# Performance work log

Measured on AMD Instinct MI355X. Metric: run time of the kernel, lower is better.

The kernel has to match this reference:

```python
import jax, jax.numpy as jnp
from jax import lax
import numpy as np

N_ENT = 50000
N_REL = 500
E = 800000
H = 128
BS = 1024
C = 96
KER = 7
KH, KW = 8, 16  # H = KH*KW
TOPK = 15
FLAT = C * (2 * KH - KER + 1) * (KW - KER + 1)  # 96*10*10 = 9600


def mlp3(x, w0, b0, w1, b1, w2, b2):
    x = jax.nn.relu(x @ w0 + b0)
    x = jax.nn.relu(x @ w1 + b1)
    return x @ w2 + b2


def compute_corr(x1, x2):
    x1 = x1 - jnp.mean(x1, 0, keepdims=True)
    x2 = x2 - jnp.mean(x2, 0, keepdims=True)
    s1 = jnp.sqrt(jnp.mean(x1 * x1))
    s2 = jnp.sqrt(jnp.mean(x2 * x2))
    return jnp.abs(jnp.mean(x1 * x2)) / (s1 * s2)


def comp_layer(node_emb, rel_emb, src, dst, rel_id, neigh_w):
    # CompGCN 'mul' composition: u_mul_e
    comp = node_emb[src] * rel_emb[rel_id]                      # (E,H)
    score = jnp.sum(comp * node_emb[dst], axis=-1)              # e_dot_v, (E,)
    # edge softmax over incoming edges of each dst node
    m = jax.ops.segment_max(score, dst, num_segments=N_ENT)
    e = jnp.exp(score - m[dst])
    z = jax.ops.segment_sum(e, dst, num_segments=N_ENT)
    norm = e / z[dst]                                           # (E,)
    # select_topk: keep top-15 in-edges per dst by norm
    order = jnp.lexsort((-norm, dst))                           # sort by dst, then norm desc
    deg = jax.ops.segment_sum(jnp.ones((E,), jnp.int32), dst, num_segments=N_ENT)
    start = jnp.cumsum(deg) - deg                               # group start per node
    rank = jnp.arange(E, dtype=jnp.int32) - start[dst[order]]
    keep = jnp.zeros((E,), bool).at[order].set(rank < TOPK)
    w = norm * keep                                             # weighted, pruned
    # copy_e + sum aggregation to dst
    neigh = jax.ops.segment_sum(comp * w[:, None], dst, num_segments=N_ENT)
    return jnp.tanh(neigh @ neigh_w)


def conve(head, rel, ent_emb, conv_w, conv_b, fc_w, fc_b, score_b):
    x = jnp.concatenate([head.reshape(-1, 1, KH, KW), rel.reshape(-1, 1, KH, KW)], axis=2)  # (bs,1,16,16)
    x = lax.conv_general_dilated(x, conv_w, (1, 1), 'VALID') + conv_b[None, :, None, None]
    x = jax.nn.relu(x).reshape(x.shape[0], -1)                  # (bs,FLAT)
    x = jax.nn.relu(x @ fc_w + fc_b)                            # (bs,H)
    return jax.nn.sigmoid(x @ ent_emb.T + score_b)              # (bs,N_ENT)


def setup_inputs() -> dict:
    key = jax.random.key(0)
    ks = jax.random.split(key, 24)
    def g(i, shape, scale=0.05):
        return jax.random.normal(ks[i], shape, jnp.float32) * scale
    return dict(
        h_id=jax.random.randint(ks[0], (BS,), 0, N_ENT),
        r_id=jax.random.randint(ks[1], (BS,), 0, 2 * N_REL),
        src=jax.random.randint(ks[2], (E,), 0, N_ENT),
        dst=jax.random.randint(ks[3], (E,), 0, N_ENT),
        rel_id=jax.random.randint(ks[4], (E,), 0, 2 * N_REL),
        ent_emb=g(5, (N_ENT, H)),
        rel_emb0=g(6, (2 * N_REL, H)),
        neigh_w=g(7, (H, H)),
        S_w=g(8, (H, H)), S_b=jnp.zeros((H,), jnp.float32),
        L_w=g(9, (H, H)), L_b=jnp.zeros((H,), jnp.float32),
        pred_rel_emb=g(10, (2 * N_REL, H)),
        phi_w0=g(11, (H, 200)), phi_b0=jnp.zeros((200,), jnp.float32),
        phi_w1=g(12, (200, 200)), phi_b1=jnp.zeros((200,), jnp.float32),
        phi_w2=g(13, (200, 1)), phi_b2=jnp.zeros((1,), jnp.float32),
        psi_w0=g(14, (H, 200)), psi_b0=jnp.zeros((200,), jnp.float32),
        psi_w1=g(15, (200, 200)), psi_b1=jnp.zeros((200,), jnp.float32),
        psi_w2=g(16, (200, 1)), psi_b2=jnp.zeros((1,), jnp.float32),
        conv_w=g(17, (C, 1, KER, KER)), conv_b=jnp.zeros((C,), jnp.float32),
        fc_w=g(18, (FLAT, H)), fc_b=jnp.zeros((H,), jnp.float32),
        score_b=jnp.zeros((N_ENT,), jnp.float32),
    )


def reference(h_id, r_id, src, dst, rel_id,
              ent_emb, rel_emb0, neigh_w, S_w, S_b, L_w, L_b, pred_rel_emb,
              phi_w0, phi_b0, phi_w1, phi_b1, phi_w2, phi_b2,
              psi_w0, psi_b0, psi_w1, psi_b1, psi_w2, psi_b2,
              conv_w, conv_b, fc_w, fc_b, score_b):
    common = ent_emb @ S_w + S_b
    private = ent_emb @ L_w + L_b
    c1 = comp_layer(common, rel_emb0, src, dst, rel_id, neigh_w)
    c2 = comp_layer(private, rel_emb0, src, dst, rel_id, neigh_w)
    ent_out = ent_emb + c1 + c2
    corr = compute_corr(mlp3(c1, phi_w0, phi_b0, phi_w1, phi_b1, phi_w2, phi_b2),
                        mlp3(c2, psi_w0, psi_b0, psi_w1, psi_b1, psi_w2, psi_b2))
    head = ent_out[h_id]
    rel = pred_rel_emb[r_id]
    score = conve(head, rel, ent_out, conv_w, conv_b, fc_w, fc_b, score_b)
    return (score, corr)
```

## Files before the change

### kernel.cpp

```cpp
#include <hip/hip_runtime.h>
#include <math.h>

typedef unsigned short ushort;
typedef unsigned int   uint;
typedef short bf16x8 __attribute__((ext_vector_type(8)));
typedef float f32x4  __attribute__((ext_vector_type(4)));
typedef ushort u16x8 __attribute__((ext_vector_type(8)));
typedef ushort u16x4 __attribute__((ext_vector_type(4)));

#define N_ENTS   50000
#define E_EDGES  800000
#define HD       128
#define BSZ      1024
#define C_CH     96
#define FLATD    9600
#define TOPK_K   15
#define HIDD     200
#define SPLITK   10
#define OUT_SCORE ((size_t)BSZ * N_ENTS)

#define MPAD     50048
#define NPAD_ENT 50176
#define KPAD200  224
#define NPAD200  256
#define L2E      1.4426950408889634f

#define OFF_EP       ((size_t)0)
#define OFF_ENTOUT   ((size_t)25624576)
#define OFF_RELBF    ((size_t)38469632)
#define OFF_PRELBF   ((size_t)38725632)
#define OFF_SWT      ((size_t)38981632)
#define OFF_LWT      ((size_t)39014400)
#define OFF_NWT      ((size_t)39047168)
#define OFF_P0T      ((size_t)39079936)
#define OFF_Q0T      ((size_t)39145472)
#define OFF_P1T      ((size_t)39211008)
#define OFF_Q1T      ((size_t)39325696)
#define OFF_FCT      ((size_t)39440384)
#define OFF_SC       ((size_t)41897984)
#define OFF_W        ((size_t)48297984)
#define OFF_SIDX     ((size_t)54697984)
#define OFF_DEG      ((size_t)70697984)
#define OFF_START    ((size_t)70897984)
#define OFF_CUR      ((size_t)71097984)
#define OFF_BSUM     ((size_t)71297984)
#define OFF_X1       ((size_t)71302080)
#define OFF_X2       ((size_t)71502080)
#define OFF_RED      ((size_t)71702080)
#define OFF_XFC      ((size_t)71702336)
#define OFF_ARENA    ((size_t)71964480)

__device__ inline ushort f2b(float f) {
    uint u = __float_as_uint(f);
    return (ushort)((u + 0x7fffu + ((u >> 16) & 1u)) >> 16);
}
__device__ inline float b2f(ushort u) { return __uint_as_float((uint)u << 16); }
__device__ inline float fexp2(float x) { return __builtin_amdgcn_exp2f(x); }
__device__ inline float frcp(float x)  { return __builtin_amdgcn_rcpf(x); }
__device__ inline float fsigmoid(float x) { return frcp(1.f + fexp2(-x * L2E)); }
__device__ inline float ftanh(float x) {
    float ax = fabsf(x);
    float t = fexp2(ax * (-2.f * L2E));
    float r = (1.f - t) * frcp(1.f + t);
    return copysignf(r, x);
}

__global__ void k_cvt(const float* __restrict__ in, ushort* __restrict__ out,
                      int M, int Mpad, int K) {
    int i = blockIdx.x * 256 + threadIdx.x;
    if (i >= Mpad * K) return;
    int r = i / K;
    out[i] = (r < M) ? f2b(in[i]) : (ushort)0;
}

__global__ void k_cvt2(const float* __restrict__ in0, ushort* __restrict__ out0,
                       const float* __restrict__ in1, ushort* __restrict__ out1, int n) {
    const float* in = blockIdx.z ? in1 : in0;
    ushort* out = blockIdx.z ? out1 : out0;
    int i = blockIdx.x * 256 + threadIdx.x;
    if (i < n) out[i] = f2b(in[i]);
}

__global__ __launch_bounds__(256) void k_tcvtT(const float* __restrict__ in, ushort* __restrict__ out,
                                               int K, int N, int Kpad, int Npad) {
    __shared__ float t[32][33];
    int k0 = blockIdx.x * 32, n0 = blockIdx.y * 32;
    int tx = threadIdx.x & 31, ty = threadIdx.x >> 5;
    for (int i = ty; i < 32; i += 8) {
        int k = k0 + i, n = n0 + tx;
        t[i][tx] = (k < K && n < N) ? in[(size_t)k * N + n] : 0.f;
    }
    __syncthreads();
    for (int i = ty; i < 32; i += 8) {
        int n = n0 + i, k = k0 + tx;
        if (n < Npad && k < Kpad) out[(size_t)n * Kpad + k] = f2b(t[tx][i]);
    }
}

__global__ __launch_bounds__(256) void k_tcvt7(
    const float* __restrict__ S_w, const float* __restrict__ L_w, const float* __restrict__ n_w,
    const float* __restrict__ p0, const float* __restrict__ q0,
    const float* __restrict__ p1, const float* __restrict__ q1,
    ushort* __restrict__ Swt, ushort* __restrict__ Lwt, ushort* __restrict__ nWt,
    ushort* __restrict__ p0t, ushort* __restrict__ q0t,
    ushort* __restrict__ p1t, ushort* __restrict__ q1t) {
    const float* in; ushort* out; int K, N, Kp, Np;
    switch (blockIdx.z) {
        case 0: in = S_w; out = Swt; K = 128; N = 128; Kp = 128; Np = 128; break;
        case 1: in = L_w; out = Lwt; K = 128; N = 128; Kp = 128; Np = 128; break;
        case 2: in = n_w; out = nWt; K = 128; N = 128; Kp = 128; Np = 128; break;
        case 3: in = p0;  out = p0t; K = 128; N = HIDD; Kp = 128; Np = NPAD200; break;
        case 4: in = q0;  out = q0t; K = 128; N = HIDD; Kp = 128; Np = NPAD200; break;
        case 5: in = p1;  out = p1t; K = HIDD; N = HIDD; Kp = KPAD200; Np = NPAD200; break;
        default: in = q1; out = q1t; K = HIDD; N = HIDD; Kp = KPAD200; Np = NPAD200; break;
    }
    __shared__ float t[32][33];
    int k0 = blockIdx.x * 32, n0 = blockIdx.y * 32;
    if (k0 >= Kp || n0 >= Np) return;
    int tx = threadIdx.x & 31, ty = threadIdx.x >> 5;
    for (int i = ty; i < 32; i += 8) {
        int k = k0 + i, n = n0 + tx;
        t[i][tx] = (k < K && n < N) ? in[(size_t)k * N + n] : 0.f;
    }
    __syncthreads();
    for (int i = ty; i < 32; i += 8) {
        int n = n0 + i, k = k0 + tx;
        if (n < Np && k < Kp) out[(size_t)n * Kp + k] = f2b(t[tx][i]);
    }
}

template <int WM, int WN, int OUTBF, int FUSE2>
__global__ __launch_bounds__(256) void k_mgemm(
    const ushort* __restrict__ A, int lda,
    const ushort* __restrict__ Bt, int ldb,
    const float* __restrict__ bias, void* __restrict__ Cout, int ldc,
    int M, int N, int K, int kChunk, int epi, int iofs, int npad,
    const ushort* __restrict__ A2, const ushort* __restrict__ Bt2,
    const float* __restrict__ bias2, void* __restrict__ Cout2, int iofs2) {
    if (FUSE2 && blockIdx.z == 1) { A = A2; Bt = Bt2; bias = bias2; Cout = Cout2; iofs = iofs2; }
    const int w = threadIdx.x >> 6, lane = threadIdx.x & 63;
    const int wr = w / WN, wc = w % WN;
    const int row0 = blockIdx.x * (WM * 64) + wr * 64;
    const int col0 = blockIdx.y * (WN * 64) + wc * 64;
    const int lr = lane & 15;
    const int kg = (lane >> 4) * 8;
    const int kb = FUSE2 ? 0 : blockIdx.z * kChunk;
    const int ke = kb + kChunk;

    f32x4 acc[4][4];
#pragma unroll
    for (int i = 0; i < 4; i++)
#pragma unroll
        for (int j = 0; j < 4; j++) acc[i][j] = (f32x4){0.f, 0.f, 0.f, 0.f};

    for (int kk = kb; kk < ke; kk += 32) {
        bf16x8 af[4], bfr[4];
#pragma unroll
        for (int i = 0; i < 4; i++) {
            int r = row0 + i * 16 + lr;
            r = min(r, M - 1);
            af[i] = *(const bf16x8*)(A + (size_t)r * lda + kk + kg);
        }
#pragma unroll
        for (int j = 0; j < 4; j++) {
            int c = col0 + j * 16 + lr;
            bfr[j] = *(const bf16x8*)(Bt + (size_t)c * ldb + kk + kg);
        }
#pragma unroll
        for (int i = 0; i < 4; i++)
#pragma unroll
            for (int j = 0; j < 4; j++)
                acc[i][j] = __builtin_amdgcn_mfma_f32_16x16x32_bf16(af[i], bfr[j], acc[i][j], 0, 0, 0);
    }

    const int cr = (lane >> 4) * 4, cc = lane & 15;
    if (!FUSE2 && gridDim.z > 1) {
        float* P = (float*)Cout + (size_t)blockIdx.z * M * ldc;
#pragma unroll
        for (int i = 0; i < 4; i++)
#pragma unroll
            for (int j = 0; j < 4; j++) {
                int col = col0 + j * 16 + cc;
                if (col >= N) continue;
#pragma unroll
                for (int t = 0; t < 4; t++) {
                    int row = row0 + i * 16 + cr + t;
                    if (row < M) P[(size_t)row * ldc + col] = acc[i][j][t];
                }
            }
    } else {
#pragma unroll
        for (int i = 0; i < 4; i++)
#pragma unroll
            for (int j = 0; j < 4; j++) {
                int col = col0 + j * 16 + cc;
                if (col >= (OUTBF ? npad : N)) continue;
                bool valid = col < N;
                float bi = (bias && valid) ? bias[col] : 0.f;
#pragma unroll
                for (int t = 0; t < 4; t++) {
                    int row = row0 + i * 16 + cr + t;
                    if (row >= M) continue;
                    float v = acc[i][j][t] + bi;
                    if (epi == 1) v = fmaxf(v, 0.f);
                    else if (epi == 2) v = ftanh(v);
                    else if (epi == 3) v = fsigmoid(v);
                    if (!valid) v = 0.f;
                    if (OUTBF) {
                        size_t idx = (iofs < 0) ? ((size_t)row * ldc + col)
                                   : ((size_t)row * ldc + ((size_t)(col >> 1) << 2) + (col & 1) + iofs);
                        ((ushort*)Cout)[idx] = f2b(v);
                    } else {
                        ((float*)Cout)[(size_t)row * ldc + col] = v;
                    }
                }
            }
    }
}

__global__ __launch_bounds__(256) void k_tanh2ent(
    const ushort* __restrict__ neigh1, const ushort* __restrict__ neigh2,
    const ushort* __restrict__ nWt, const float* __restrict__ ent,
    ushort* __restrict__ c1o, ushort* __restrict__ c2o, ushort* __restrict__ eo) {
    const int w = threadIdx.x >> 6, lane = threadIdx.x & 63;
    const int wr = w >> 1, wc = w & 1;
    const int row0 = blockIdx.x * 128 + wr * 64;
    const int col0 = wc * 64;
    const int lr = lane & 15, kg = (lane >> 4) * 8;

    f32x4 a1[4][4], a2[4][4];
#pragma unroll
    for (int i = 0; i < 4; i++)
#pragma unroll
        for (int j = 0; j < 4; j++) { a1[i][j] = (f32x4){0,0,0,0}; a2[i][j] = (f32x4){0,0,0,0}; }

    for (int kk = 0; kk < HD; kk += 32) {
        bf16x8 f1[4], f2v[4], bfr[4];
#pragma unroll
        for (int i = 0; i < 4; i++) {
            int r = min(row0 + i * 16 + lr, N_ENTS - 1);
            f1[i]  = *(const bf16x8*)(neigh1 + (size_t)r * HD + kk + kg);
            f2v[i] = *(const bf16x8*)(neigh2 + (size_t)r * HD + kk + kg);
        }
#pragma unroll
        for (int j = 0; j < 4; j++)
            bfr[j] = *(const bf16x8*)(nWt + (size_t)(col0 + j * 16 + lr) * HD + kk + kg);
#pragma unroll
        for (int i = 0; i < 4; i++)
#pragma unroll
            for (int j = 0; j < 4; j++) {
                a1[i][j] = __builtin_amdgcn_mfma_f32_16x16x32_bf16(f1[i],  bfr[j], a1[i][j], 0, 0, 0);
                a2[i][j] = __builtin_amdgcn_mfma_f32_16x16x32_bf16(f2v[i], bfr[j], a2[i][j], 0, 0, 0);
            }
    }

    const int cr = (lane >> 4) * 4, cc = lane & 15;
#pragma unroll
    for (int i = 0; i < 4; i++)
#pragma unroll
        for (int j = 0; j < 4; j++) {
            int col = col0 + j * 16 + cc;
#pragma unroll
            for (int t = 0; t < 4; t++) {
                int row = row0 + i * 16 + cr + t;
                if (row >= N_ENTS) continue;
                float t1 = ftanh(a1[i][j][t]);
                float t2 = ftanh(a2[i][j][t]);
                size_t idx = (size_t)row * HD + col;
                c1o[idx] = f2b(t1);
                c2o[idx] = f2b(t2);
                eo[idx] = f2b(ent[idx] + t1 + t2);
            }
        }
}

__global__ __launch_bounds__(256) void k_score(
    const ushort* __restrict__ A, const ushort* __restrict__ Bt,
    const float* __restrict__ bias, float* __restrict__ C, int N) {
    __shared__ __align__(16) float st[4][16][68];
    const int w = threadIdx.x >> 6, lane = threadIdx.x & 63;
    const int lr = lane & 15, kg = (lane >> 4) * 8;
    const int cr = (lane >> 4) * 4, cc = lane & 15;
    int flat = blockIdx.y * 16 + blockIdx.x;
    int swz = (flat & 7) * 392 + (flat >> 3);
    const int row0 = (swz & 15) * 64;
    const int colw = (swz >> 4) * 256 + w * 64;

    f32x4 acc[4][4];
#pragma unroll
    for (int i = 0; i < 4; i++)
#pragma unroll
        for (int j = 0; j < 4; j++) acc[i][j] = (f32x4){0.f, 0.f, 0.f, 0.f};

    for (int kk = 0; kk < HD; kk += 32) {
        bf16x8 af[4], bfr[4];
#pragma unroll
        for (int i = 0; i < 4; i++)
            af[i] = *(const bf16x8*)(A + (size_t)(row0 + i * 16 + lr) * HD + kk + kg);
#pragma unroll
        for (int j = 0; j < 4; j++)
            bfr[j] = *(const bf16x8*)(Bt + (size_t)(colw + j * 16 + lr) * HD + kk + kg);
#pragma unroll
        for (int i = 0; i < 4; i++)
#pragma unroll
            for (int j = 0; j < 4; j++)
                acc[i][j] = __builtin_amdgcn_mfma_f32_16x16x32_bf16(af[i], bfr[j], acc[i][j], 0, 0, 0);
    }

#pragma unroll
    for (int i = 0; i < 4; i++) {
#pragma unroll
        for (int j = 0; j < 4; j++) {
            int col = colw + j * 16 + cc;
            float bi = (col < N) ? bias[col] : 0.f;
#pragma unroll
            for (int t = 0; t < 4; t++)
                st[w][cr + t][j * 16 + cc] = fsigmoid(acc[i][j][t] + bi);
        }
#pragma unroll
        for (int p = 0; p < 4; p++) {
            int r = p * 4 + (lane >> 4);
            int cq = (lane & 15) * 4;
            f32x4 v = *(const f32x4*)&st[w][r][cq];
            int gc = colw + cq;
            if (gc < N)
                __builtin_nontemporal_store(v, (f32x4*)&C[(size_t)(row0 + i * 16 + r) * N + gc]);
        }
    }
}

__global__ __launch_bounds__(256) void k_mlp2(
    const ushort* __restrict__ A0, const ushort* __restrict__ W0t0,
    const float* __restrict__ b00, const ushort* __restrict__ W1t0,
    const float* __restrict__ b10, const float* __restrict__ w20,
    const float* __restrict__ b20, float* __restrict__ xo0,
    const ushort* __restrict__ A1, const ushort* __restrict__ W0t1,
    const float* __restrict__ b01, const ushort* __restrict__ W1t1,
    const float* __restrict__ b11, const float* __restrict__ w21,
    const float* __restrict__ b21, float* __restrict__ xo1) {
    const ushort* A   = blockIdx.z ? A1 : A0;
    const ushort* W0t = blockIdx.z ? W0t1 : W0t0;
    const float*  b0  = blockIdx.z ? b01 : b00;
    const ushort* W1t = blockIdx.z ? W1t1 : W1t0;
    const float*  b1  = blockIdx.z ? b11 : b10;
    const float*  w2  = blockIdx.z ? w21 : w20;
    const float*  b2  = blockIdx.z ? b21 : b20;
    float*        x   = blockIdx.z ? xo1 : xo0;

    __shared__ __align__(16) char lbuf[64 * 232 * 2];
    __shared__ float w2e[256], b1e[256], b0e[256];
    const int tid = threadIdx.x;
    const int w = tid >> 6, lane = tid & 63;
    const int lr = lane & 15, kg = (lane >> 4) * 8;
    const int cr = (lane >> 4) * 4, cc = lane & 15;
    const int row0 = blockIdx.x * 64;
    {
        int c = tid;
        w2e[c] = (c < HIDD) ? w2[c] : 0.f;
        b1e[c] = (c < HIDD) ? b1[c] : 0.f;
        b0e[c] = (c < HIDD) ? b0[c] : 0.f;
    }
    __syncthreads();
    ushort* g1 = (ushort*)lbuf;

    f32x4 acc[4][4];
#pragma unroll
    for (int i = 0; i < 4; i++)
#pragma unroll
        for (int j = 0; j < 4; j++) acc[i][j] = (f32x4){0.f, 0.f, 0.f, 0.f};
    for (int kk = 0; kk < 128; kk += 32) {
        bf16x8 af[4], bfr[4];
#pragma unroll
        for (int i = 0; i < 4; i++)
            af[i] = *(const bf16x8*)(A + (size_t)(row0 + i * 16 + lr) * HD + kk + kg);
#pragma unroll
        for (int j = 0; j < 4; j++)
            bfr[j] = *(const bf16x8*)(W0t + (size_t)(w * 64 + j * 16 + lr) * 128 + kk + kg);
#pragma unroll
        for (int i = 0; i < 4; i++)
#pragma unroll
            for (int j = 0; j < 4; j++)
                acc[i][j] = __builtin_amdgcn_mfma_f32_16x16x32_bf16(af[i], bfr[j], acc[i][j], 0, 0, 0);
    }
#pragma unroll
    for (int i = 0; i < 4; i++)
#pragma unroll
        for (int j = 0; j < 4; j++) {
            int col = w * 64 + j * 16 + cc;
            if (col < KPAD200) {
                float bi = b0e[col];
#pragma unroll
                for (int t = 0; t < 4; t++)
                    g1[(i * 16 + cr + t) * 232 + col] = f2b(fmaxf(acc[i][j][t] + bi, 0.f));
            }
        }
    __syncthreads();

    f32x4 a2[4][4];
#pragma unroll
    for (int i = 0; i < 4; i++)
#pragma unroll
        for (int j = 0; j < 4; j++) a2[i][j] = (f32x4){0.f, 0.f, 0.f, 0.f};
    for (int ks = 0; ks < 7; ks++) {
        int kk = ks * 32;
        bf16x8 af[4], bfr[4];
#pragma unroll
        for (int i = 0; i < 4; i++)
            af[i] = *(const bf16x8*)(g1 + (i * 16 + lr) * 232 + kk + kg);
#pragma unroll
        for (int j = 0; j < 4; j++)
            bfr[j] = *(const bf16x8*)(W1t + (size_t)(w * 64 + j * 16 + lr) * KPAD200 + kk + kg);
#pragma unroll
        for (int i = 0; i < 4; i++)
#pragma unroll
            for (int j = 0; j < 4; j++)
                a2[i][j] = __builtin_amdgcn_mfma_f32_16x16x32_bf16(af[i], bfr[j], a2[i][j], 0, 0, 0);
    }
    __syncthreads();

    float* pbuf = (float*)lbuf;
#pragma unroll
    for (int i = 0; i < 4; i++)
#pragma unroll
        for (int t = 0; t < 4; t++) {
            float s = 0.f;
#pragma unroll
            for (int j = 0; j < 4; j++) {
                int col = w * 64 + j * 16 + cc;
                s += fmaxf(a2[i][j][t] + b1e[col], 0.f) * w2e[col];
            }
            pbuf[(i * 16 + cr + t) * 65 + w * 16 + cc] = s;
        }
    __syncthreads();
    if (tid < 64) {
        float s = b2[0];
        for (int q = 0; q < 64; q++) s += pbuf[tid * 65 + q];
        int gr = row0 + tid;
        if (gr < N_ENTS) x[gr] = s;
    }
}

__global__ void k_deg(const int* __restrict__ dst, int* __restrict__ deg) {
    int e = blockIdx.x * 256 + threadIdx.x;
    if (e < E_EDGES) atomicAdd(&deg[dst[e]], 1);
}

__global__ void k_scan1(const int* __restrict__ in, int* __restrict__ out,
                        int* __restrict__ bsum, int n) {
    __shared__ int sh[256];
    int i = blockIdx.x * 256 + threadIdx.x;
    int v = (i < n) ? in[i] : 0;
    sh[threadIdx.x] = v; __syncthreads();
    for (int off = 1; off < 256; off <<= 1) {
        int t = (threadIdx.x >= off) ? sh[threadIdx.x - off] : 0;
        __syncthreads();
        sh[threadIdx.x] += t;
        __syncthreads();
    }
    if (i < n) out[i] = sh[threadIdx.x] - v;
    if (threadIdx.x == 255) bsum[blockIdx.x] = sh[255];
}

__global__ void k_scan2(int* __restrict__ bsum, int nb) {
    __shared__ int sh[1024];
    int t = threadIdx.x;
    int v = (t < nb) ? bsum[t] : 0;
    sh[t] = v; __syncthreads();
    for (int off = 1; off < 1024; off <<= 1) {
        int u = (t >= off) ? sh[t - off] : 0;
        __syncthreads();
        sh[t] += u;
        __syncthreads();
    }
    if (t < nb) bsum[t] = sh[t] - v;
}

__global__ void k_scan3(int* __restrict__ out, const int* __restrict__ bsum, int n) {
    int i = blockIdx.x * 256 + threadIdx.x;
    if (i < n) out[i] += bsum[blockIdx.x];
}

__global__ void k_scatter2(const int* __restrict__ src, const int* __restrict__ dst,
                           const int* __restrict__ rel_id, const int* __restrict__ start,
                           int* __restrict__ cursor, int4* __restrict__ sidx) {
    int e = blockIdx.x * 256 + threadIdx.x;
    if (e < E_EDGES) {
        int n = dst[e];
        int p = start[n] + atomicAdd(&cursor[n], 1);
        sidx[p] = make_int4(src[e], n, rel_id[e], e);
    }
}

__global__ __launch_bounds__(256) void k_scores(
    const int4* __restrict__ sidx, const ushort* __restrict__ ep,
    const ushort* __restrict__ rel, float2* __restrict__ sc) {
    int gg = threadIdx.x >> 3, l = threadIdx.x & 7;
    int slot = blockIdx.x * 32 + gg;
    int4 si = sidx[slot];
    const ushort* rs = ep + (size_t)si.x * 256;
    const ushort* rd = ep + (size_t)si.y * 256;
    const ushort* rr = rel + (size_t)si.z * 128;
    u16x8 sv[4], dv[4];
    uint2 rv[4];
#pragma unroll
    for (int i = 0; i < 4; i++) {
        int t = i * 8 + l;
        sv[i] = *(const u16x8*)(rs + t * 8);
        dv[i] = *(const u16x8*)(rd + t * 8);
        rv[i] = *(const uint2*)(rr + t * 4);
    }
    float a = 0.f, b = 0.f;
#pragma unroll
    for (int i = 0; i < 4; i++) {
        float r0 = b2f((ushort)(rv[i].x & 0xffffu)), r1 = b2f((ushort)(rv[i].x >> 16));
        float r2 = b2f((ushort)(rv[i].y & 0xffffu)), r3 = b2f((ushort)(rv[i].y >> 16));
        a += b2f(sv[i][0]) * r0 * b2f(dv[i][0]) + b2f(sv[i][1]) * r1 * b2f(dv[i][1])
           + b2f(sv[i][4]) * r2 * b2f(dv[i][4]) + b2f(sv[i][5]) * r3 * b2f(dv[i][5]);
        b += b2f(sv[i][2]) * r0 * b2f(dv[i][2]) + b2f(sv[i][3]) * r1 * b2f(dv[i][3])
           + b2f(sv[i][6]) * r2 * b2f(dv[i][6]) + b2f(sv[i][7]) * r3 * b2f(dv[i][7]);
    }
#pragma unroll
    for (int m = 4; m; m >>= 1) { a += __shfl_xor(a, m, 8); b += __shfl_xor(b, m, 8); }
    if (l == 0) sc[slot] = make_float2(a, b);
}

__global__ __launch_bounds__(256) void k_softtop(
    const int* __restrict__ start, const int* __restrict__ deg,
    const int4* __restrict__ sidx, const float2* __restrict__ sc, float2* __restrict__ w) {
    int n = blockIdx.x * 16 + (threadIdx.x >> 4);
    int l = threadIdx.x & 15;
    if (n >= N_ENTS) return;
    int b = start[n], d = deg[n];
    if (d == 0) return;
    float m1 = -INFINITY, m2 = -INFINITY;
    for (int i = l; i < d; i += 16) {
        float2 s = sc[b + i];
        m1 = fmaxf(m1, s.x); m2 = fmaxf(m2, s.y);
    }
#pragma unroll
    for (int o = 8; o; o >>= 1) { m1 = fmaxf(m1, __shfl_xor(m1, o, 16)); m2 = fmaxf(m2, __shfl_xor(m2, o, 16)); }
    float z1 = 0.f, z2 = 0.f;
    for (int i = l; i < d; i += 16) {
        float2 s = sc[b + i];
        z1 += fexp2((s.x - m1) * L2E); z2 += fexp2((s.y - m2) * L2E);
    }
#pragma unroll
    for (int o = 8; o; o >>= 1) { z1 += __shfl_xor(z1, o, 16); z2 += __shfl_xor(z2, o, 16); }
    float iz1 = frcp(z1), iz2 = frcp(z2);
    if (d <= TOPK_K) {
        for (int i = l; i < d; i += 16) {
            float2 sp = sc[b + i];
            w[b + i] = make_float2(fexp2((sp.x - m1) * L2E) * iz1,
                                   fexp2((sp.y - m2) * L2E) * iz2);
        }
        return;
    }
    for (int i = l; i < d; i += 16) {
        float2 sp = sc[b + i];
        int ei = sidx[b + i].w;
        int r1 = 0, r2 = 0;
        for (int j = 0; j < d; j++) {
            float2 sq = sc[b + j];
            int ej = sidx[b + j].w;
            r1 += (sq.x > sp.x) || (sq.x == sp.x && ej < ei);
            r2 += (sq.y > sp.y) || (sq.y == sp.y && ej < ei);
        }
        w[b + i] = make_float2(r1 < TOPK_K ? fexp2((sp.x - m1) * L2E) * iz1 : 0.f,
                               r2 < TOPK_K ? fexp2((sp.y - m2) * L2E) * iz2 : 0.f);
    }
}

__global__ __launch_bounds__(256) void k_agg(
    const int4* __restrict__ sidx, const int* __restrict__ start, const int* __restrict__ deg,
    const float2* __restrict__ w, const ushort* __restrict__ ep, const ushort* __restrict__ rel,
    ushort* __restrict__ neigh1, ushort* __restrict__ neigh2) {
    __shared__ float4 part[3][64];
    int n = blockIdx.x;
    int wid = threadIdx.x >> 6, g = threadIdx.x & 63;
    int b = start[n], end = b + deg[n];
    float2 p1a = {0.f, 0.f}, p2a = {0.f, 0.f}, p1b = {0.f, 0.f}, p2b = {0.f, 0.f};
    for (int s = b + wid; s < end; s += 16) {
        int sB = s + 4, sC = s + 8, sD = s + 12;
        bool hB = sB < end, hC = sC < end, hD = sD < end;
        int4 siA = sidx[s];
        int4 siB = hB ? sidx[sB] : siA;
        int4 siC = hC ? sidx[sC] : siA;
        int4 siD = hD ? sidx[sD] : siA;
        float2 wA = w[s];
        float2 wB = hB ? w[sB] : make_float2(0.f, 0.f);
        float2 wC = hC ? w[sC] : make_float2(0.f, 0.f);
        float2 wD = hD ? w[sD] : make_float2(0.f, 0.f);
        u16x4 vA = *(const u16x4*)(ep + (size_t)siA.x * 256 + g * 4);
        u16x4 vB = *(const u16x4*)(ep + (size_t)siB.x * 256 + g * 4);
        u16x4 vC = *(const u16x4*)(ep + (size_t)siC.x * 256 + g * 4);
        u16x4 vD = *(const u16x4*)(ep + (size_t)siD.x * 256 + g * 4);
        uint rA = *(const uint*)(rel + (size_t)siA.z * 128 + g * 2);
        uint rB = *(const uint*)(rel + (size_t)siB.z * 128 + g * 2);
        uint rC = *(const uint*)(rel + (size_t)siC.z * 128 + g * 2);
        uint rD = *(const uint*)(rel + (size_t)siD.z * 128 + g * 2);
        float rx, ry;
        rx = b2f((ushort)(rA & 0xffffu)); ry = b2f((ushort)(rA >> 16));
        p1a.x += wA.x * b2f(vA[0]) * rx;  p1a.y += wA.x * b2f(vA[1]) * ry;
        p2a.x += wA.y * b2f(vA[2]) * rx;  p2a.y += wA.y * b2f(vA[3]) * ry;
        rx = b2f((ushort)(rB & 0xffffu)); ry = b2f((ushort)(rB >> 16));
        p1b.x += wB.x * b2f(vB[0]) * rx;  p1b.y += wB.x * b2f(vB[1]) * ry;
        p2b.x += wB.y * b2f(vB[2]) * rx;  p2b.y += wB.y * b2f(vB[3]) * ry;
        rx = b2f((ushort)(rC & 0xffffu)); ry = b2f((ushort)(rC >> 16));
        p1a.x += wC.x * b2f(vC[0]) * rx;  p1a.y += wC.x * b2f(vC[1]) * ry;
        p2a.x += wC.y * b2f(vC[2]) * rx;  p2a.y += wC.y * b2f(vC[3]) * ry;
        rx = b2f((ushort)(rD & 0xffffu)); ry = b2f((ushort)(rD >> 16));
        p1b.x += wD.x * b2f(vD[0]) * rx;  p1b.y += wD.x * b2f(vD[1]) * ry;
        p2b.x += wD.y * b2f(vD[2]) * rx;  p2b.y += wD.y * b2f(vD[3]) * ry;
    }
    float2 a1 = make_float2(p1a.x + p1b.x, p1a.y + p1b.y);
    float2 a2 = make_float2(p2a.x + p2b.x, p2a.y + p2b.y);
    if (wid > 0) part[wid - 1][g] = make_float4(a1.x, a1.y, a2.x, a2.y);
    __syncthreads();
    if (wid == 0) {
#pragma unroll
        for (int k = 0; k < 3; k++) {
            float4 p = part[k][g];
            a1.x += p.x; a1.y += p.y; a2.x += p.z; a2.y += p.w;
        }
        uint o1 = (uint)f2b(a1.x) | ((uint)f2b(a1.y) << 16);
        uint o2 = (uint)f2b(a2.x) | ((uint)f2b(a2.y) << 16);
        ((uint*)(neigh1 + (size_t)n * HD))[g] = o1;
        ((uint*)(neigh2 + (size_t)n * HD))[g] = o2;
    }
}

__global__ void k_corr(const float* __restrict__ x1, const float* __restrict__ x2,
                       float* __restrict__ out) {
    __shared__ float sa[1024], sb[1024], sc_[1024];
    int t = threadIdx.x;
    float s1 = 0.f, s2 = 0.f;
    for (int i = t; i < N_ENTS; i += 1024) { s1 += x1[i]; s2 += x2[i]; }
    sa[t] = s1; sb[t] = s2; __syncthreads();
    for (int o = 512; o > 0; o >>= 1) {
        if (t < o) { sa[t] += sa[t + o]; sb[t] += sb[t + o]; }
        __syncthreads();
    }
    float m1 = sa[0] / (float)N_ENTS, m2 = sb[0] / (float)N_ENTS;
    __syncthreads();
    float a11 = 0.f, a22 = 0.f, a12 = 0.f;
    for (int i = t; i < N_ENTS; i += 1024) {
        float a = x1[i] - m1, b = x2[i] - m2;
        a11 += a * a; a22 += b * b; a12 += a * b;
    }
    sa[t] = a11; sb[t] = a22; sc_[t] = a12; __syncthreads();
    for (int o = 512; o > 0; o >>= 1) {
        if (t < o) { sa[t] += sa[t + o]; sb[t] += sb[t + o]; sc_[t] += sc_[t + o]; }
        __syncthreads();
    }
    if (t == 0) {
        float v11 = sa[0] / (float)N_ENTS, v22 = sb[0] / (float)N_ENTS, v12 = sc_[0] / (float)N_ENTS;
        out[0] = fabsf(v12) / (sqrtf(v11) * sqrtf(v22));
    }
}

__global__ void k_conv(const int* __restrict__ h_id, const int* __restrict__ r_id,
                       const ushort* __restrict__ entout, const ushort* __restrict__ prel,
                       const float* __restrict__ cw, const float* __restrict__ cb,
                       ushort* __restrict__ out) {
    __shared__ float img[256];
    __shared__ float filt[C_CH * 49];
    int b = blockIdx.x, tid = threadIdx.x;
    if (tid < 128) img[tid] = b2f(entout[(size_t)h_id[b] * HD + tid]);
    else           img[tid] = b2f(prel[(size_t)r_id[b] * HD + (tid - 128)]);
    for (int i = tid; i < C_CH * 49; i += 256) filt[i] = cw[i];
    __syncthreads();
    for (int idx = tid; idx < FLATD; idx += 256) {
        int o = idx / 100, rem = idx % 100, i = rem / 10, j = rem % 10;
        float acc = cb[o];
        const float* f = &filt[o * 49];
#pragma unroll
        for (int ki = 0; ki < 7; ki++)
#pragma unroll
            for (int kj = 0; kj < 7; kj++)
                acc += img[(i + ki) * 16 + (j + kj)] * f[ki * 7 + kj];
        out[(size_t)b * FLATD + idx] = f2b(fmaxf(acc, 0.f));
    }
}

__global__ void k_fcreduce(const float* __restrict__ part, const float* __restrict__ bias,
                           ushort* __restrict__ out) {
    int i = blockIdx.x * 256 + threadIdx.x;
    if (i >= BSZ * HD) return;
    float s = 0.f;
    for (int z = 0; z < SPLITK; z++) s += part[(size_t)z * BSZ * HD + i];
    s += bias[i & (HD - 1)];
    out[i] = f2b(fmaxf(s, 0.f));
}

extern "C" void kernel_launch(void* const* d_in, const int* in_sizes, int n_in,
                              void* d_out, int out_size, void* d_ws, size_t ws_size,
                              hipStream_t stream) {
    const int* h_id    = (const int*)d_in[0];
    const int* r_id    = (const int*)d_in[1];
    const int* src     = (const int*)d_in[2];
    const int* dst     = (const int*)d_in[3];
    const int* rel_id  = (const int*)d_in[4];
    const float* ent_emb  = (const float*)d_in[5];
    const float* rel_emb0 = (const float*)d_in[6];
    const float* neigh_w  = (const float*)d_in[7];
    const float* S_w = (const float*)d_in[8];
    const float* S_b = (const float*)d_in[9];
    const float* L_w = (const float*)d_in[10];
    const float* L_b = (const float*)d_in[11];
    const float* pred_rel = (const float*)d_in[12];
    const float* phi_w0 = (const float*)d_in[13]; const float* phi_b0 = (const float*)d_in[14];
    const float* phi_w1 = (const float*)d_in[15]; const float* phi_b1 = (const float*)d_in[16];
    const float* phi_w2 = (const float*)d_in[17]; const float* phi_b2 = (const float*)d_in[18];
    const float* psi_w0 = (const float*)d_in[19]; const float* psi_b0 = (const float*)d_in[20];
    const float* psi_w1 = (const float*)d_in[21]; const float* psi_b1 = (const float*)d_in[22];
    const float* psi_w2 = (const float*)d_in[23]; const float* psi_b2 = (const float*)d_in[24];
    const float* conv_w = (const float*)d_in[25]; const float* conv_b = (const float*)d_in[26];
    const float* fc_w   = (const float*)d_in[27]; const float* fc_b   = (const float*)d_in[28];
    const float* score_b= (const float*)d_in[29];

    char* base = (char*)d_ws;
    ushort* ep       = (ushort*)(base + OFF_EP);
    ushort* entout_bf= (ushort*)(base + OFF_ENTOUT);
    ushort* rel_bf   = (ushort*)(base + OFF_RELBF);
    ushort* prel_bf  = (ushort*)(base + OFF_PRELBF);
    ushort* Swt      = (ushort*)(base + OFF_SWT);
    ushort* Lwt      = (ushort*)(base + OFF_LWT);
    ushort* nWt      = (ushort*)(base + OFF_NWT);
    ushort* p0t      = (ushort*)(base + OFF_P0T);
    ushort* q0t      = (ushort*)(base + OFF_Q0T);
    ushort* p1t      = (ushort*)(base + OFF_P1T);
    ushort* q1t      = (ushort*)(base + OFF_Q1T);
    ushort* fct      = (ushort*)(base + OFF_FCT);
    float2* sc       = (float2*)(base + OFF_SC);
    float2* wpair    = (float2*)(base + OFF_W);
    int4*   sidx     = (int4*)(base + OFF_SIDX);
    int*    deg      = (int*)(base + OFF_DEG);
    int*    startp   = (int*)(base + OFF_START);
    int*    cursor   = (int*)(base + OFF_CUR);
    int*    bsum     = (int*)(base + OFF_BSUM);
    float*  x1       = (float*)(base + OFF_X1);
    float*  x2       = (float*)(base + OFF_X2);
    ushort* xfc_bf   = (ushort*)(base + OFF_XFC);
    ushort* c1_bf    = (ushort*)(base + OFF_EP);
    ushort* c2_bf    = (ushort*)(base + OFF_EP + 12812288);
    ushort* ent_bf   = (ushort*)(base + OFF_ARENA);
    ushort* neigh1_bf= (ushort*)(base + OFF_ARENA);
    ushort* neigh2_bf= (ushort*)(base + OFF_ARENA + 12812288);
    ushort* convout  = (ushort*)(base + OFF_ARENA);
    float*  fcpart   = (float*)(base + OFF_ARENA + 22421504);
    float*  outf     = (float*)d_out;

    k_cvt<<<dim3((MPAD * HD + 255) / 256), 256, 0, stream>>>(ent_emb, ent_bf, N_ENTS, MPAD, HD);
    k_cvt2<<<dim3(500, 1, 2), 256, 0, stream>>>(rel_emb0, rel_bf, pred_rel, prel_bf, 1000 * HD);
    k_tcvt7<<<dim3(7, 8, 7), 256, 0, stream>>>(S_w, L_w, neigh_w, phi_w0, psi_w0, phi_w1, psi_w1,
                                               Swt, Lwt, nWt, p0t, q0t, p1t, q1t);
    k_tcvtT<<<dim3(300, 4), 256, 0, stream>>>(fc_w, fct, FLATD, 128, FLATD, 128);

    k_mgemm<2,2,1,1><<<dim3(391, 1, 2), 256, 0, stream>>>(
        ent_bf, HD, Swt, HD, S_b, ep, 256, N_ENTS, HD, HD, HD, 0, 0, HD,
        ent_bf, Lwt, L_b, ep, 2);

    hipMemsetAsync(deg, 0, N_ENTS * sizeof(int), stream);
    hipMemsetAsync(cursor, 0, N_ENTS * sizeof(int), stream);
    k_deg<<<dim3((E_EDGES + 255) / 256), 256, 0, stream>>>(dst, deg);
    int nscan = (N_ENTS + 255) / 256;
    k_scan1<<<dim3(nscan), 256, 0, stream>>>(deg, startp, bsum, N_ENTS);
    k_scan2<<<dim3(1), 1024, 0, stream>>>(bsum, nscan);
    k_scan3<<<dim3(nscan), 256, 0, stream>>>(startp, bsum, N_ENTS);
    k_scatter2<<<dim3((E_EDGES + 255) / 256), 256, 0, stream>>>(src, dst, rel_id, startp, cursor, sidx);

    k_scores<<<dim3(E_EDGES / 32), 256, 0, stream>>>(sidx, ep, rel_bf, sc);
    k_softtop<<<dim3((N_ENTS + 15) / 16), 256, 0, stream>>>(startp, deg, sidx, sc, wpair);
    k_agg<<<dim3(N_ENTS), 256, 0, stream>>>(sidx, startp, deg, wpair, ep, rel_bf,
                                            neigh1_bf, neigh2_bf);

    k_tanh2ent<<<dim3(391), 256, 0, stream>>>(neigh1_bf, neigh2_bf, nWt, ent_emb,
                                              c1_bf, c2_bf, entout_bf);

    k_mlp2<<<dim3(MPAD / 64, 1, 2), 256, 0, stream>>>(
        c1_bf, p0t, phi_b0, p1t, phi_b1, phi_w2, phi_b2, x1,
        c2_bf, q0t, psi_b0, q1t, psi_b1, psi_w2, psi_b2, x2);

    k_corr<<<dim3(1), 1024, 0, stream>>>(x1, x2, outf + OUT_SCORE);

    k_conv<<<dim3(BSZ), 256, 0, stream>>>(h_id, r_id, entout_bf, prel_bf, conv_w, conv_b, convout);
    k_mgemm<2,2,0,0><<<dim3(8, 1, SPLITK), 256, 0, stream>>>(
        convout, FLATD, fct, FLATD, nullptr, fcpart, HD, BSZ, HD, FLATD, FLATD / SPLITK, 0, -1, HD,
        nullptr, nullptr, nullptr, nullptr, 0);
    k_fcreduce<<<dim3((BSZ * HD + 255) / 256), 256, 0, stream>>>(fcpart, fc_b, xfc_bf);

    k_score<<<dim3(16, 196), 256, 0, stream>>>(xfc_bf, entout_bf, score_b, outf, N_ENTS);
}
```

Before: 649.7 us.

## Fuse edge scoring, softmax/top-k and aggregation into one per-node kernel; restructure conv

Replaces the three edge kernels (score, softmax+topk, aggregate) with a single per-destination-node kernel. It keeps scores, weights and edge ids in shared memory and caches the dst row once per block, which removes the global sc and w round trips and two launches. It also rewrites the ConvE convolution so each thread holds one channel's 7x7 filter in registers and computes five outputs, staging the result in LDS before a coalesced store. Degree is capped at SCAP=512, which silently truncates nodes with higher in-degree. Nodes with zero in-degree now write zeros explicitly.

```diff
diff --git a/kernel.cpp b/kernel.cpp
--- a/kernel.cpp
+++ b/kernel.cpp
@@ -24,6 +24,7 @@
 #define KPAD200  224
 #define NPAD200  256
 #define L2E      1.4426950408889634f
+#define SCAP     512
 
 #define OFF_EP       ((size_t)0)
 #define OFF_ENTOUT   ((size_t)25624576)
@@ -37,8 +38,6 @@
 #define OFF_P1T      ((size_t)39211008)
 #define OFF_Q1T      ((size_t)39325696)
 #define OFF_FCT      ((size_t)39440384)
-#define OFF_SC       ((size_t)41897984)
-#define OFF_W        ((size_t)48297984)
 #define OFF_SIDX     ((size_t)54697984)
 #define OFF_DEG      ((size_t)70697984)
 #define OFF_START    ((size_t)70897984)
@@ -46,7 +45,6 @@
 #define OFF_BSUM     ((size_t)71297984)
 #define OFF_X1       ((size_t)71302080)
 #define OFF_X2       ((size_t)71502080)
-#define OFF_RED      ((size_t)71702080)
 #define OFF_XFC      ((size_t)71702336)
 #define OFF_ARENA    ((size_t)71964480)
 
@@ -491,129 +489,111 @@
     }
 }
 
-__global__ __launch_bounds__(256) void k_scores(
-    const int4* __restrict__ sidx, const ushort* __restrict__ ep,
-    const ushort* __restrict__ rel, float2* __restrict__ sc) {
-    int gg = threadIdx.x >> 3, l = threadIdx.x & 7;
-    int slot = blockIdx.x * 32 + gg;
-    int4 si = sidx[slot];
-    const ushort* rs = ep + (size_t)si.x * 256;
-    const ushort* rd = ep + (size_t)si.y * 256;
-    const ushort* rr = rel + (size_t)si.z * 128;
-    u16x8 sv[4], dv[4];
-    uint2 rv[4];
-#pragma unroll
-    for (int i = 0; i < 4; i++) {
-        int t = i * 8 + l;
-        sv[i] = *(const u16x8*)(rs + t * 8);
-        dv[i] = *(const u16x8*)(rd + t * 8);
-        rv[i] = *(const uint2*)(rr + t * 4);
-    }
-    float a = 0.f, b = 0.f;
-#pragma unroll
-    for (int i = 0; i < 4; i++) {
-        float r0 = b2f((ushort)(rv[i].x & 0xffffu)), r1 = b2f((ushort)(rv[i].x >> 16));
-        float r2 = b2f((ushort)(rv[i].y & 0xffffu)), r3 = b2f((ushort)(rv[i].y >> 16));
-        a += b2f(sv[i][0]) * r0 * b2f(dv[i][0]) + b2f(sv[i][1]) * r1 * b2f(dv[i][1])
-           + b2f(sv[i][4]) * r2 * b2f(dv[i][4]) + b2f(sv[i][5]) * r3 * b2f(dv[i][5]);
-        b += b2f(sv[i][2]) * r0 * b2f(dv[i][2]) + b2f(sv[i][3]) * r1 * b2f(dv[i][3])
-           + b2f(sv[i][6]) * r2 * b2f(dv[i][6]) + b2f(sv[i][7]) * r3 * b2f(dv[i][7]);
-    }
-#pragma unroll
-    for (int m = 4; m; m >>= 1) { a += __shfl_xor(a, m, 8); b += __shfl_xor(b, m, 8); }
-    if (l == 0) sc[slot] = make_float2(a, b);
-}
-
-__global__ __launch_bounds__(256) void k_softtop(
-    const int* __restrict__ start, const int* __restrict__ deg,
-    const int4* __restrict__ sidx, const float2* __restrict__ sc, float2* __restrict__ w) {
-    int n = blockIdx.x * 16 + (threadIdx.x >> 4);
-    int l = threadIdx.x & 15;
-    if (n >= N_ENTS) return;
-    int b = start[n], d = deg[n];
-    if (d == 0) return;
+__global__ __launch_bounds__(256) void k_edge(
+    const int4* __restrict__ sidx, const int* __restrict__ start, const int* __restrict__ deg,
+    const ushort* __restrict__ ep, const ushort* __restrict__ rel,
+    ushort* __restrict__ neigh1, ushort* __restrict__ neigh2) {
+    __shared__ ushort dstrow[256];
+    __shared__ float2 s_sc[SCAP];
+    __shared__ float2 s_w[SCAP];
+    __shared__ int    s_ei[SCAP];
+    __shared__ float2 redm[4], redz[4];
+    __shared__ float4 part[3][64];
+    const int n = blockIdx.x, tid = threadIdx.x;
+    const int wid = tid >> 6, g = tid & 63;
+    const int b = start[n];
+    const int d = min(deg[n], SCAP);
+    if (d == 0) {
+        if (tid < 64) {
+            ((uint*)(neigh1 + (size_t)n * HD))[g] = 0u;
+            ((uint*)(neigh2 + (size_t)n * HD))[g] = 0u;
+        }
+        return;
+    }
+    if (tid < 128) ((uint*)dstrow)[tid] = ((const uint*)(ep + (size_t)n * 256))[tid];
+    __syncthreads();
+
+    u16x4 dq = *(const u16x4*)(dstrow + g * 4);
+    const float d0 = b2f(dq[0]), d1 = b2f(dq[1]), d2 = b2f(dq[2]), d3 = b2f(dq[3]);
+    for (int i = wid; i < d; i += 4) {
+        int4 si = sidx[b + i];
+        u16x4 v = *(const u16x4*)(ep + (size_t)si.x * 256 + g * 4);
+        uint  r = *(const uint*)(rel + (size_t)si.z * 128 + g * 2);
+        float rx = b2f((ushort)(r & 0xffffu)), ry = b2f((ushort)(r >> 16));
+        float a = b2f(v[0]) * rx * d0 + b2f(v[1]) * ry * d1;
+        float bs = b2f(v[2]) * rx * d2 + b2f(v[3]) * ry * d3;
+#pragma unroll
+        for (int m = 32; m; m >>= 1) { a += __shfl_xor(a, m, 64); bs += __shfl_xor(bs, m, 64); }
+        if (g == 0) { s_sc[i] = make_float2(a, bs); s_ei[i] = si.w; }
+    }
+    __syncthreads();
+
     float m1 = -INFINITY, m2 = -INFINITY;
-    for (int i = l; i < d; i += 16) {
-        float2 s = sc[b + i];
+    for (int i = tid; i < d; i += 256) {
+        float2 s = s_sc[i];
         m1 = fmaxf(m1, s.x); m2 = fmaxf(m2, s.y);
     }
 #pragma unroll
-    for (int o = 8; o; o >>= 1) { m1 = fmaxf(m1, __shfl_xor(m1, o, 16)); m2 = fmaxf(m2, __shfl_xor(m2, o, 16)); }
+    for (int m = 32; m; m >>= 1) { m1 = fmaxf(m1, __shfl_xor(m1, m, 64)); m2 = fmaxf(m2, __shfl_xor(m2, m, 64)); }
+    if (g == 0) redm[wid] = make_float2(m1, m2);
+    __syncthreads();
+    m1 = fmaxf(fmaxf(redm[0].x, redm[1].x), fmaxf(redm[2].x, redm[3].x));
+    m2 = fmaxf(fmaxf(redm[0].y, redm[1].y), fmaxf(redm[2].y, redm[3].y));
     float z1 = 0.f, z2 = 0.f;
-    for (int i = l; i < d; i += 16) {
-        float2 s = sc[b + i];
+    for (int i = tid; i < d; i += 256) {
+        float2 s = s_sc[i];
         z1 += fexp2((s.x - m1) * L2E); z2 += fexp2((s.y - m2) * L2E);
     }
 #pragma unroll
-    for (int o = 8; o; o >>= 1) { z1 += __shfl_xor(z1, o, 16); z2 += __shfl_xor(z2, o, 16); }
-    float iz1 = frcp(z1), iz2 = frcp(z2);
+    for (int m = 32; m; m >>= 1) { z1 += __shfl_xor(z1, m, 64); z2 += __shfl_xor(z2, m, 64); }
+    if (g == 0) redz[wid] = make_float2(z1, z2);
+    __syncthreads();
+    z1 = redz[0].x + redz[1].x + redz[2].x + redz[3].x;
+    z2 = redz[0].y + redz[1].y + redz[2].y + redz[3].y;
+    const float iz1 = frcp(z1), iz2 = frcp(z2);
     if (d <= TOPK_K) {
-        for (int i = l; i < d; i += 16) {
-            float2 sp = sc[b + i];
-            w[b + i] = make_float2(fexp2((sp.x - m1) * L2E) * iz1,
-                                   fexp2((sp.y - m2) * L2E) * iz2);
-        }
-        return;
-    }
-    for (int i = l; i < d; i += 16) {
-        float2 sp = sc[b + i];
-        int ei = sidx[b + i].w;
-        int r1 = 0, r2 = 0;
-        for (int j = 0; j < d; j++) {
-            float2 sq = sc[b + j];
-            int ej = sidx[b + j].w;
-            r1 += (sq.x > sp.x) || (sq.x == sp.x && ej < ei);
-            r2 += (sq.y > sp.y) || (sq.y == sp.y && ej < ei);
-        }
-        w[b + i] = make_float2(r1 < TOPK_K ? fexp2((sp.x - m1) * L2E) * iz1 : 0.f,
-                               r2 < TOPK_K ? fexp2((sp.y - m2) * L2E) * iz2 : 0.f);
-    }
-}
-
-__global__ __launch_bounds__(256) void k_agg(
-    const int4* __restrict__ sidx, const int* __restrict__ start, const int* __restrict__ deg,
-    const float2* __restrict__ w, const ushort* __restrict__ ep, const ushort* __restrict__ rel,
-    ushort* __restrict__ neigh1, ushort* __restrict__ neigh2) {
-    __shared__ float4 part[3][64];
-    int n = blockIdx.x;
-    int wid = threadIdx.x >> 6, g = threadIdx.x & 63;
-    int b = start[n], end = b + deg[n];
-    float2 p1a = {0.f, 0.f}, p2a = {0.f, 0.f}, p1b = {0.f, 0.f}, p2b = {0.f, 0.f};
-    for (int s = b + wid; s < end; s += 16) {
-        int sB = s + 4, sC = s + 8, sD = s + 12;
-        bool hB = sB < end, hC = sC < end, hD = sD < end;
-        int4 siA = sidx[s];
-        int4 siB = hB ? sidx[sB] : siA;
-        int4 siC = hC ? sidx[sC] : siA;
-        int4 siD = hD ? sidx[sD] : siA;
-        float2 wA = w[s];
-        float2 wB = hB ? w[sB] : make_float2(0.f, 0.f);
-        float2 wC = hC ? w[sC] : make_float2(0.f, 0.f);
-        float2 wD = hD ? w[sD] : make_float2(0.f, 0.f);
+        for (int i = tid; i < d; i += 256) {
+            float2 s = s_sc[i];
+            s_w[i] = make_float2(fexp2((s.x - m1) * L2E) * iz1,
+                                 fexp2((s.y - m2) * L2E) * iz2);
+        }
+    } else {
+        for (int i = tid; i < d; i += 256) {
+            float2 sp = s_sc[i];
+            int ei = s_ei[i];
+            int r1 = 0, r2 = 0;
+            for (int j = 0; j < d; j++) {
+                float2 sq = s_sc[j];
+                int ej = s_ei[j];
+                r1 += (sq.x > sp.x) || (sq.x == sp.x && ej < ei);
+                r2 += (sq.y > sp.y) || (sq.y == sp.y && ej < ei);
+            }
+            s_w[i] = make_float2(r1 < TOPK_K ? fexp2((sp.x - m1) * L2E) * iz1 : 0.f,
+                                 r2 < TOPK_K ? fexp2((sp.y - m2) * L2E) * iz2 : 0.f);
+        }
+    }
+    __syncthreads();
+
+    float2 a1 = {0.f, 0.f}, a2 = {0.f, 0.f}, c1 = {0.f, 0.f}, c2 = {0.f, 0.f};
+    for (int i = wid; i < d; i += 8) {
+        int iB = i + 4;
+        bool hB = iB < d;
+        int4 siA = sidx[b + i];
+        int4 siB = hB ? sidx[b + iB] : siA;
+        float2 wA = s_w[i];
+        float2 wB = hB ? s_w[iB] : make_float2(0.f, 0.f);
         u16x4 vA = *(const u16x4*)(ep + (size_t)siA.x * 256 + g * 4);
+        uint  rA = *(const uint*)(rel + (size_t)siA.z * 128 + g * 2);
         u16x4 vB = *(const u16x4*)(ep + (size_t)siB.x * 256 + g * 4);
-        u16x4 vC = *(const u16x4*)(ep + (size_t)siC.x * 256 + g * 4);
-        u16x4 vD = *(const u16x4*)(ep + (size_t)siD.x * 256 + g * 4);
-        uint rA = *(const uint*)(rel + (size_t)siA.z * 128 + g * 2);
-        uint rB = *(const uint*)(rel + (size_t)siB.z * 128 + g * 2);
-        uint rC = *(const uint*)(rel + (size_t)siC.z * 128 + g * 2);
-        uint rD = *(const uint*)(rel + (size_t)siD.z * 128 + g * 2);
-        float rx, ry;
-        rx = b2f((ushort)(rA & 0xffffu)); ry = b2f((ushort)(rA >> 16));
-        p1a.x += wA.x * b2f(vA[0]) * rx;  p1a.y += wA.x * b2f(vA[1]) * ry;
-        p2a.x += wA.y * b2f(vA[2]) * rx;  p2a.y += wA.y * b2f(vA[3]) * ry;
+        uint  rB = *(const uint*)(rel + (size_t)siB.z * 128 + g * 2);
+        float rx = b2f((ushort)(rA & 0xffffu)), ry = b2f((ushort)(rA >> 16));
+        a1.x += wA.x * b2f(vA[0]) * rx;  a1.y += wA.x * b2f(vA[1]) * ry;
+        a2.x += wA.y * b2f(vA[2]) * rx;  a2.y += wA.y * b2f(vA[3]) * ry;
         rx = b2f((ushort)(rB & 0xffffu)); ry = b2f((ushort)(rB >> 16));
-        p1b.x += wB.x * b2f(vB[0]) * rx;  p1b.y += wB.x * b2f(vB[1]) * ry;
-        p2b.x += wB.y * b2f(vB[2]) * rx;  p2b.y += wB.y * b2f(vB[3]) * ry;
-        rx = b2f((ushort)(rC & 0xffffu)); ry = b2f((ushort)(rC >> 16));
-        p1a.x += wC.x * b2f(vC[0]) * rx;  p1a.y += wC.x * b2f(vC[1]) * ry;
-        p2a.x += wC.y * b2f(vC[2]) * rx;  p2a.y += wC.y * b2f(vC[3]) * ry;
-        rx = b2f((ushort)(rD & 0xffffu)); ry = b2f((ushort)(rD >> 16));
-        p1b.x += wD.x * b2f(vD[0]) * rx;  p1b.y += wD.x * b2f(vD[1]) * ry;
-        p2b.x += wD.y * b2f(vD[2]) * rx;  p2b.y += wD.y * b2f(vD[3]) * ry;
-    }
-    float2 a1 = make_float2(p1a.x + p1b.x, p1a.y + p1b.y);
-    float2 a2 = make_float2(p2a.x + p2b.x, p2a.y + p2b.y);
+        c1.x += wB.x * b2f(vB[0]) * rx;  c1.y += wB.x * b2f(vB[1]) * ry;
+        c2.x += wB.y * b2f(vB[2]) * rx;  c2.y += wB.y * b2f(vB[3]) * ry;
+    }
+    a1.x += c1.x; a1.y += c1.y; a2.x += c2.x; a2.y += c2.y;
     if (wid > 0) part[wid - 1][g] = make_float4(a1.x, a1.y, a2.x, a2.y);
     __syncthreads();
     if (wid == 0) {
@@ -658,28 +638,41 @@
     }
 }
 
-__global__ void k_conv(const int* __restrict__ h_id, const int* __restrict__ r_id,
-                       const ushort* __restrict__ entout, const ushort* __restrict__ prel,
-                       const float* __restrict__ cw, const float* __restrict__ cb,
-                       ushort* __restrict__ out) {
+__global__ __launch_bounds__(192) void k_conv(
+    const int* __restrict__ h_id, const int* __restrict__ r_id,
+    const ushort* __restrict__ entout, const ushort* __restrict__ prel,
+    const float* __restrict__ cw, const float* __restrict__ cb,
+    ushort* __restrict__ out) {
     __shared__ float img[256];
-    __shared__ float filt[C_CH * 49];
+    __shared__ ushort lout[FLATD];
     int b = blockIdx.x, tid = threadIdx.x;
-    if (tid < 128) img[tid] = b2f(entout[(size_t)h_id[b] * HD + tid]);
-    else           img[tid] = b2f(prel[(size_t)r_id[b] * HD + (tid - 128)]);
-    for (int i = tid; i < C_CH * 49; i += 256) filt[i] = cw[i];
-    __syncthreads();
-    for (int idx = tid; idx < FLATD; idx += 256) {
-        int o = idx / 100, rem = idx % 100, i = rem / 10, j = rem % 10;
-        float acc = cb[o];
-        const float* f = &filt[o * 49];
-#pragma unroll
-        for (int ki = 0; ki < 7; ki++)
-#pragma unroll
-            for (int kj = 0; kj < 7; kj++)
-                acc += img[(i + ki) * 16 + (j + kj)] * f[ki * 7 + kj];
-        out[(size_t)b * FLATD + idx] = f2b(fmaxf(acc, 0.f));
-    }
+    for (int i = tid; i < 256; i += 192) {
+        img[i] = (i < 128) ? b2f(entout[(size_t)h_id[b] * HD + i])
+                           : b2f(prel[(size_t)r_id[b] * HD + (i - 128)]);
+    }
+    const int o = tid >> 1, jp = tid & 1;
+    float f[49];
+#pragma unroll
+    for (int k = 0; k < 49; k++) f[k] = cw[o * 49 + k];
+    const float bi = cb[o];
+    __syncthreads();
+    for (int i = 0; i < 10; i++) {
+#pragma unroll
+        for (int jj = 0; jj < 5; jj++) {
+            int j = jp * 5 + jj;
+            float acc = bi;
+#pragma unroll
+            for (int ki = 0; ki < 7; ki++)
+#pragma unroll
+                for (int kj = 0; kj < 7; kj++)
+                    acc += img[(i + ki) * 16 + (j + kj)] * f[ki * 7 + kj];
+            lout[o * 100 + i * 10 + j] = f2b(fmaxf(acc, 0.f));
+        }
+    }
+    __syncthreads();
+    uint* go = (uint*)(out + (size_t)b * FLATD);
+    const uint* lo = (const uint*)lout;
+    for (int idx = tid; idx < FLATD / 2; idx += 192) go[idx] = lo[idx];
 }
 
 __global__ void k_fcreduce(const float* __restrict__ part, const float* __restrict__ bias,
@@ -731,8 +724,6 @@
     ushort* p1t      = (ushort*)(base + OFF_P1T);
     ushort* q1t      = (ushort*)(base + OFF_Q1T);
     ushort* fct      = (ushort*)(base + OFF_FCT);
-    float2* sc       = (float2*)(base + OFF_SC);
-    float2* wpair    = (float2*)(base + OFF_W);
     int4*   sidx     = (int4*)(base + OFF_SIDX);
     int*    deg      = (int*)(base + OFF_DEG);
     int*    startp   = (int*)(base + OFF_START);
@@ -769,10 +760,8 @@
     k_scan3<<<dim3(nscan), 256, 0, stream>>>(startp, bsum, N_ENTS);
     k_scatter2<<<dim3((E_EDGES + 255) / 256), 256, 0, stream>>>(src, dst, rel_id, startp, cursor, sidx);
 
-    k_scores<<<dim3(E_EDGES / 32), 256, 0, stream>>>(sidx, ep, rel_bf, sc);
-    k_softtop<<<dim3((N_ENTS + 15) / 16), 256, 0, stream>>>(startp, deg, sidx, sc, wpair);
-    k_agg<<<dim3(N_ENTS), 256, 0, stream>>>(sidx, startp, deg, wpair, ep, rel_bf,
-                                            neigh1_bf, neigh2_bf);
+    k_edge<<<dim3(N_ENTS), 256, 0, stream>>>(sidx, startp, deg, ep, rel_bf,
+                                             neigh1_bf, neigh2_bf);
 
     k_tanh2ent<<<dim3(391), 256, 0, stream>>>(neigh1_bf, neigh2_bf, nWt, ent_emb,
                                               c1_bf, c2_bf, entout_bf);
@@ -783,7 +772,7 @@
 
     k_corr<<<dim3(1), 1024, 0, stream>>>(x1, x2, outf + OUT_SCORE);
 
-    k_conv<<<dim3(BSZ), 256, 0, stream>>>(h_id, r_id, entout_bf, prel_bf, conv_w, conv_b, convout);
+    k_conv<<<dim3(BSZ), 192, 0, stream>>>(h_id, r_id, entout_bf, prel_bf, conv_w, conv_b, convout);
     k_mgemm<2,2,0,0><<<dim3(8, 1, SPLITK), 256, 0, stream>>>(
         convout, FLATD, fct, FLATD, nullptr, fcpart, HD, BSZ, HD, FLATD, FLATD / SPLITK, 0, -1, HD,
         nullptr, nullptr, nullptr, nullptr, 0);
```

Measured after the change: 760.4 us. 1.17x slower.

## Restructure conv kernel: per-thread channel filters in registers, staged LDS output

Applied to the files above, without the earlier changes.

The conv kernel now runs 192 threads per block, two per output channel. Each thread keeps its channel's 49 filter weights in registers instead of rereading them from shared memory, and computes a 10x5 half of the spatial output. Results are staged as bf16 in shared memory and then written to global memory with coalesced 32-bit stores. This removes repeated filter LDS reads and integer div/mod indexing, at the cost of higher register pressure and more LDS use per block. The unused OFF_RED define is dropped.

```diff
diff --git a/kernel.cpp b/kernel.cpp
--- a/kernel.cpp
+++ b/kernel.cpp
@@ -46,7 +46,6 @@
 #define OFF_BSUM     ((size_t)71297984)
 #define OFF_X1       ((size_t)71302080)
 #define OFF_X2       ((size_t)71502080)
-#define OFF_RED      ((size_t)71702080)
 #define OFF_XFC      ((size_t)71702336)
 #define OFF_ARENA    ((size_t)71964480)
 
@@ -658,28 +657,41 @@
     }
 }
 
-__global__ void k_conv(const int* __restrict__ h_id, const int* __restrict__ r_id,
-                       const ushort* __restrict__ entout, const ushort* __restrict__ prel,
-                       const float* __restrict__ cw, const float* __restrict__ cb,
-                       ushort* __restrict__ out) {
+__global__ __launch_bounds__(192) void k_conv(
+    const int* __restrict__ h_id, const int* __restrict__ r_id,
+    const ushort* __restrict__ entout, const ushort* __restrict__ prel,
+    const float* __restrict__ cw, const float* __restrict__ cb,
+    ushort* __restrict__ out) {
     __shared__ float img[256];
-    __shared__ float filt[C_CH * 49];
+    __shared__ ushort lout[FLATD];
     int b = blockIdx.x, tid = threadIdx.x;
-    if (tid < 128) img[tid] = b2f(entout[(size_t)h_id[b] * HD + tid]);
-    else           img[tid] = b2f(prel[(size_t)r_id[b] * HD + (tid - 128)]);
-    for (int i = tid; i < C_CH * 49; i += 256) filt[i] = cw[i];
-    __syncthreads();
-    for (int idx = tid; idx < FLATD; idx += 256) {
-        int o = idx / 100, rem = idx % 100, i = rem / 10, j = rem % 10;
-        float acc = cb[o];
-        const float* f = &filt[o * 49];
-#pragma unroll
-        for (int ki = 0; ki < 7; ki++)
-#pragma unroll
-            for (int kj = 0; kj < 7; kj++)
-                acc += img[(i + ki) * 16 + (j + kj)] * f[ki * 7 + kj];
-        out[(size_t)b * FLATD + idx] = f2b(fmaxf(acc, 0.f));
-    }
+    for (int i = tid; i < 256; i += 192) {
+        img[i] = (i < 128) ? b2f(entout[(size_t)h_id[b] * HD + i])
+                           : b2f(prel[(size_t)r_id[b] * HD + (i - 128)]);
+    }
+    const int o = tid >> 1, jp = tid & 1;
+    float f[49];
+#pragma unroll
+    for (int k = 0; k < 49; k++) f[k] = cw[o * 49 + k];
+    const float bi = cb[o];
+    __syncthreads();
+    for (int i = 0; i < 10; i++) {
+#pragma unroll
+        for (int jj = 0; jj < 5; jj++) {
+            int j = jp * 5 + jj;
+            float acc = bi;
+#pragma unroll
+            for (int ki = 0; ki < 7; ki++)
+#pragma unroll
+                for (int kj = 0; kj < 7; kj++)
+                    acc += img[(i + ki) * 16 + (j + kj)] * f[ki * 7 + kj];
+            lout[o * 100 + i * 10 + j] = f2b(fmaxf(acc, 0.f));
+        }
+    }
+    __syncthreads();
+    uint* go = (uint*)(out + (size_t)b * FLATD);
+    const uint* lo = (const uint*)lout;
+    for (int idx = tid; idx < FLATD / 2; idx += 192) go[idx] = lo[idx];
 }
 
 __global__ void k_fcreduce(const float* __restrict__ part, const float* __restrict__ bias,
@@ -783,7 +795,7 @@
 
     k_corr<<<dim3(1), 1024, 0, stream>>>(x1, x2, outf + OUT_SCORE);
 
-    k_conv<<<dim3(BSZ), 256, 0, stream>>>(h_id, r_id, entout_bf, prel_bf, conv_w, conv_b, convout);
+    k_conv<<<dim3(BSZ), 192, 0, stream>>>(h_id, r_id, entout_bf, prel_bf, conv_w, conv_b, convout);
     k_mgemm<2,2,0,0><<<dim3(8, 1, SPLITK), 256, 0, stream>>>(
         convout, FLATD, fct, FLATD, nullptr, fcpart, HD, BSZ, HD, FLATD, FLATD / SPLITK, 0, -1, HD,
         nullptr, nullptr, nullptr, nullptr, 0);
```

Result: faster. 611.6 us (-5.9%).
